# Performance work log

Hardware: AMD Instinct MI355X
Metric: run time of the kernel (lower is better)

Reference implementation:

```python
import jax, jax.numpy as jnp
import numpy as np

V = 33279   # num_tokens
E = 256     # embedding_size
H = 512     # hidden_size
NH = 8      # num_heads
L = 4       # num_layers
DH = E // NH
MAXPOS = 64


def _ln(x, g, b):
    mu = jnp.mean(x, axis=-1, keepdims=True)
    var = jnp.mean((x - mu) ** 2, axis=-1, keepdims=True)
    return (x - mu) / jnp.sqrt(var + 1e-5) * g + b


def setup_inputs() -> dict:
    key = jax.random.key(0)
    ks = jax.random.split(key, 32)
    N, S = 128, 64
    label = jax.random.randint(ks[0], (N, S), 0, V)
    # Bernoulli(0.15) BERT-style mask (deterministic stand-in for torch sampling)
    mask = (jax.random.uniform(ks[1], (N, S)) < 0.15).astype(jnp.int32)
    s = 0.02
    inp = {
        'label': label, 'mask': mask,
        'emb': jax.random.normal(ks[2], (V + 1, E)) * s,
        'pos': jax.random.normal(ks[3], (MAXPOS, E)) * s,
        'emb_g': jnp.ones((E,)), 'emb_b': jnp.zeros((E,)),
        # stacked per-layer params (leading dim L)
        'Wq': jax.random.normal(ks[4], (L, E, E)) * s, 'bq': jnp.zeros((L, E)),
        'Wk': jax.random.normal(ks[5], (L, E, E)) * s, 'bk': jnp.zeros((L, E)),
        'Wv': jax.random.normal(ks[6], (L, E, E)) * s, 'bv': jnp.zeros((L, E)),
        'Wo': jax.random.normal(ks[7], (L, E, E)) * s, 'bo': jnp.zeros((L, E)),
        'n1g': jnp.ones((L, E)), 'n1b': jnp.zeros((L, E)),
        'W1': jax.random.normal(ks[8], (L, E, H)) * s, 'b1': jnp.zeros((L, H)),
        'W2': jax.random.normal(ks[9], (L, H, E)) * s, 'b2': jnp.zeros((L, E)),
        'n2g': jnp.ones((L, E)), 'n2b': jnp.zeros((L, E)),
        # decoder head
        'dW1': jax.random.normal(ks[10], (E, E)) * s, 'db1': jnp.zeros((E,)),
        'dng': jnp.ones((E,)), 'dnb': jnp.zeros((E,)),
        'dW2': jax.random.normal(ks[11], (E, V)) * s, 'db2': jnp.zeros((V,)),
    }
    return inp


def reference(label, mask, emb, pos, emb_g, emb_b, Wq, bq, Wk, bk, Wv, bv,
              Wo, bo, n1g, n1b, W1, b1, W2, b2, n2g, n2b,
              dW1, db1, dng, dnb, dW2, db2):
    N, S = label.shape
    src_ids = jnp.where(mask == 1, V, label)  # masked-token id = num_tokens
    # embedding + positional, then LayerNorm (eval: Scaler/Dropout identity)
    x = emb[src_ids] + pos[:S][None, :, :]
    x = _ln(x, emb_g, emb_b)
    temp = jnp.asarray((E // NH) ** 0.5, x.dtype)

    def layer(x, p):
        wq, bq_, wk, bk_, wv, bv_, wo, bo_, g1, b1n, w1, b1_, w2, b2_, g2, b2n = p
        q = (x @ wq + bq_).reshape(N, S, NH, DH).transpose(0, 2, 1, 3)
        k = (x @ wk + bk_).reshape(N, S, NH, DH).transpose(0, 2, 1, 3)
        v = (x @ wv + bv_).reshape(N, S, NH, DH).transpose(0, 2, 1, 3)
        scores = jnp.einsum('nhsd,nhtd->nhst', q, k) / temp
        attn = jax.nn.softmax(scores, axis=-1)
        o = jnp.einsum('nhst,nhtd->nhsd', attn, v)
        o = o.transpose(0, 2, 1, 3).reshape(N, S, E) @ wo + bo_
        x1 = _ln(x + o, g1, b1n)
        ff = jax.nn.gelu(x1 @ w1 + b1_, approximate=False) @ w2 + b2_
        x2 = _ln(x1 + ff, g2, b2n)
        return x2, None

    x, _ = jax.lax.scan(layer, x, (Wq, bq, Wk, bk, Wv, bv, Wo, bo,
                                   n1g, n1b, W1, b1, W2, b2, n2g, n2b))
    # decoder head: linear -> gelu -> LN -> vocab projection
    h = jax.nn.gelu(x @ dW1 + db1, approximate=False)
    h = _ln(h, dng, dnb)
    logits = h @ dW2 + db2               # [N, S, V]
    logp = jax.nn.log_softmax(logits, axis=-1)
    loss = -jnp.take_along_axis(logp, label[..., None], axis=-1).mean()
    score = logits.transpose(0, 2, 1)    # [N, V, S] like torch permute(0,2,1)
    return score, loss
```

## Files before the change

### kernel.cpp

```cpp
#include <hip/hip_runtime.h>
#include <hip/hip_bf16.h>

#define DEVFN static __device__ __forceinline__

constexpr int N_ = 128, S_ = 64, T_ = N_ * S_;
constexpr int E_ = 256, H_ = 512, NH_ = 8, DH_ = 32, L_ = 4;
constexpr int V_ = 33279, VPAD_ = 33280, NVT_ = VPAD_ / 256;

typedef __attribute__((ext_vector_type(8))) short bf16x8;
typedef __attribute__((ext_vector_type(4))) float f32x4;
typedef unsigned short ushort_t;

DEVFN ushort_t f2bf(float f) {
  unsigned int u = __float_as_uint(f);
  unsigned int r = (u + 0x7fffu + ((u >> 16) & 1u)) >> 16;
  return (ushort_t)r;
}
DEVFN float bf2f(ushort_t u) { return __uint_as_float(((unsigned)u) << 16); }

DEVFN float geluf(float x) {
  return 0.5f * x * (1.f + erff(x * 0.70710678118654752440f));
}

DEVFN float wave_sum(float v) {
  #pragma unroll
  for (int off = 32; off >= 1; off >>= 1) v += __shfl_xor(v, off, 64);
  return v;
}

DEVFN float l15_sum(float v) {
  v += __shfl_xor(v, 1, 64);
  v += __shfl_xor(v, 2, 64);
  v += __shfl_xor(v, 4, 64);
  v += __shfl_xor(v, 8, 64);
  return v;
}

__global__ __launch_bounds__(256) void k_embed_ln(
    const int* __restrict__ label, const int* __restrict__ mask,
    const float* __restrict__ emb, const float* __restrict__ pos,
    const float* __restrict__ g, const float* __restrict__ b,
    float* __restrict__ x, ushort_t* __restrict__ xb) {
  int wv = threadIdx.x >> 6, lane = threadIdx.x & 63;
  int t = blockIdx.x * 4 + wv;
  int s = t & (S_ - 1);
  int id = (mask[t] == 1) ? V_ : label[t];
  int c = lane * 4;
  float4 v = *(const float4*)&emb[(size_t)id * E_ + c];
  float4 p = *(const float4*)&pos[s * E_ + c];
  v.x += p.x; v.y += p.y; v.z += p.z; v.w += p.w;
  float mean = wave_sum(v.x + v.y + v.z + v.w) * (1.f / E_);
  float4 d = {v.x - mean, v.y - mean, v.z - mean, v.w - mean};
  float var = wave_sum(d.x * d.x + d.y * d.y + d.z * d.z + d.w * d.w) * (1.f / E_);
  float rstd = 1.f / sqrtf(var + 1e-5f);
  float4 g4 = *(const float4*)&g[c];
  float4 b4 = *(const float4*)&b[c];
  float4 y = {d.x * rstd * g4.x + b4.x, d.y * rstd * g4.y + b4.y,
              d.z * rstd * g4.z + b4.z, d.w * rstd * g4.w + b4.w};
  *(float4*)&x[(size_t)t * E_ + c] = y;
  ushort4 yb = {f2bf(y.x), f2bf(y.y), f2bf(y.z), f2bf(y.w)};
  *(ushort4*)&xb[(size_t)t * E_ + c] = yb;
}

__global__ __launch_bounds__(256) void k_prep(
    const float* __restrict__ Wq, const float* __restrict__ Wk,
    const float* __restrict__ Wv, const float* __restrict__ Wo,
    const float* __restrict__ dW1, const float* __restrict__ W1,
    const float* __restrict__ W2, const float* __restrict__ bq,
    const float* __restrict__ bk, const float* __restrict__ bv,
    ushort_t* __restrict__ wqkvT, ushort_t* __restrict__ woT,
    ushort_t* __restrict__ dw1T, ushort_t* __restrict__ w1T,
    ushort_t* __restrict__ w2T, float* __restrict__ bqkv) {
  int z = blockIdx.z;
  if (z == 25) {
    if (blockIdx.x == 0 && blockIdx.y == 0) {
      for (int i = threadIdx.x; i < L_ * 768; i += 256) {
        int l = i / 768, c = i - l * 768;
        float v = (c < 256) ? bq[l * 256 + c]
                : (c < 512) ? bk[l * 256 + c - 256]
                            : bv[l * 256 + c - 512];
        bqkv[i] = v;
      }
    }
    return;
  }
  const float* src;
  ushort_t* dst;
  int K, J;
  if (z < 17) {
    if (blockIdx.x >= 8 || blockIdx.y >= 8) return;
    K = 256; J = 256;
    if (z == 16) { src = dW1; dst = dw1T; }
    else {
      int w = z >> 2, l = z & 3;
      const float* ws = (w == 0) ? Wq : (w == 1) ? Wk : (w == 2) ? Wv : Wo;
      src = ws + (size_t)l * 65536;
      dst = (w < 3) ? (wqkvT + (size_t)l * 768 * 256 + (size_t)w * 256 * 256)
                    : (woT + (size_t)l * 65536);
    }
  } else if (z < 21) {
    int l = z - 17; K = 256; J = 512;
    if (blockIdx.y >= 8) return;
    src = W1 + (size_t)l * K * J; dst = w1T + (size_t)l * J * K;
  } else {
    int l = z - 21; K = 512; J = 256;
    if (blockIdx.x >= 8) return;
    src = W2 + (size_t)l * K * J; dst = w2T + (size_t)l * J * K;
  }
  __shared__ float tile[32][33];
  int j0 = blockIdx.x * 32, k0 = blockIdx.y * 32;
  int tx = threadIdx.x & 31, ty = threadIdx.x >> 5;
  #pragma unroll
  for (int rr = 0; rr < 4; rr++) {
    int kk = ty * 4 + rr;
    tile[kk][tx] = src[(size_t)(k0 + kk) * J + j0 + tx];
  }
  __syncthreads();
  #pragma unroll
  for (int rr = 0; rr < 4; rr++) {
    int jj = ty * 4 + rr;
    dst[(size_t)(j0 + jj) * K + k0 + tx] = f2bf(tile[tx][jj]);
  }
}

template <int K, int OUT_BF16, int GELU_>
__global__ __launch_bounds__(256) void k_mm(
    const ushort_t* __restrict__ Xb, const ushort_t* __restrict__ WT,
    const float* __restrict__ bias, void* __restrict__ C, int Nout) {
  constexpr int STR = K + 8;
  __shared__ ushort_t xs[64 * STR];
  int tid = threadIdx.x, lane = tid & 63, wv = tid >> 6;
  int t0 = blockIdx.x * 64, j0 = blockIdx.y * 64;
  const ushort_t* xsrc = Xb + (size_t)t0 * K;
  for (int i = tid; i < 64 * (K / 8); i += 256) {
    int r = i / (K / 8), c = (i % (K / 8)) * 8;
    *(uint4*)&xs[r * STR + c] = *(const uint4*)&xsrc[(size_t)r * K + c];
  }
  __syncthreads();
  int l15 = lane & 15, l4 = lane >> 4;
  f32x4 acc[4] = {};
  const ushort_t* xrow = &xs[(wv * 16 + l15) * STR + l4 * 8];
  const ushort_t* wrow = WT + (size_t)j0 * K + l4 * 8;
  #pragma unroll
  for (int kb = 0; kb < K / 32; kb++) {
    bf16x8 a = *(const bf16x8*)(xrow + kb * 32);
    #pragma unroll
    for (int st = 0; st < 4; st++) {
      bf16x8 bfr = *(const bf16x8*)(wrow + (size_t)(st * 16 + l15) * K + kb * 32);
      acc[st] = __builtin_amdgcn_mfma_f32_16x16x32_bf16(a, bfr, acc[st], 0, 0, 0);
    }
  }
  #pragma unroll
  for (int st = 0; st < 4; st++) {
    int j = j0 + st * 16 + l15;
    float bv_ = bias[j];
    #pragma unroll
    for (int r = 0; r < 4; r++) {
      float val = acc[st][r] + bv_;
      if (GELU_) val = geluf(val);
      int t = t0 + wv * 16 + l4 * 4 + r;
      if (OUT_BF16)
        ((ushort_t*)C)[(size_t)t * Nout + j] = f2bf(val);
      else
        ((float*)C)[(size_t)t * Nout + j] = val;
    }
  }
}

template <int K, int GELU_PRE, int HAS_RES, int OUT_F32>
__global__ __launch_bounds__(256) void k_mm_ln2(
    const ushort_t* __restrict__ Xb, const ushort_t* __restrict__ WT,
    const float* __restrict__ bias, const float* __restrict__ res,
    const float* __restrict__ g, const float* __restrict__ bet,
    float* __restrict__ y, ushort_t* __restrict__ yb) {
  constexpr int STR = K + 8;
  __shared__ ushort_t xs[16 * STR];
  __shared__ float redA[4][16], redB[4][16];
  int tid = threadIdx.x, lane = tid & 63, wv = tid >> 6;
  int t0 = blockIdx.x * 16;
  const ushort_t* xsrc = Xb + (size_t)t0 * K;
  for (int i = tid; i < 16 * (K / 8); i += 256) {
    int r = i / (K / 8), c = (i % (K / 8)) * 8;
    *(uint4*)&xs[r * STR + c] = *(const uint4*)&xsrc[(size_t)r * K + c];
  }
  __syncthreads();
  int l15 = lane & 15, l4 = lane >> 4;
  f32x4 acc[4] = {};
  const ushort_t* xrow = &xs[l15 * STR + l4 * 8];
  const ushort_t* wrow = WT + (size_t)(wv * 64) * K + l4 * 8;
  #pragma unroll
  for (int kb = 0; kb < K / 32; kb++) {
    bf16x8 a = *(const bf16x8*)(xrow + kb * 32);
    #pragma unroll
    for (int st = 0; st < 4; st++) {
      bf16x8 bfr = *(const bf16x8*)(wrow + (size_t)(st * 16 + l15) * K + kb * 32);
      acc[st] = __builtin_amdgcn_mfma_f32_16x16x32_bf16(a, bfr, acc[st], 0, 0, 0);
    }
  }
  float val[4][4];
  #pragma unroll
  for (int st = 0; st < 4; st++) {
    int j = wv * 64 + st * 16 + l15;
    float bv_ = bias[j];
    #pragma unroll
    for (int r = 0; r < 4; r++) {
      float v = acc[st][r] + bv_;
      if (GELU_PRE) v = geluf(v);
      if (HAS_RES) v += res[(size_t)(t0 + l4 * 4 + r) * E_ + j];
      val[st][r] = v;
    }
  }
  #pragma unroll
  for (int r = 0; r < 4; r++) {
    float s = val[0][r] + val[1][r] + val[2][r] + val[3][r];
    s = l15_sum(s);
    if (l15 == 0) redA[wv][l4 * 4 + r] = s;
  }
  __syncthreads();
  float mean[4];
  #pragma unroll
  for (int r = 0; r < 4; r++) {
    int row = l4 * 4 + r;
    mean[r] = (redA[0][row] + redA[1][row] + redA[2][row] + redA[3][row]) * (1.f / E_);
  }
  #pragma unroll
  for (int r = 0; r < 4; r++) {
    float s = 0.f;
    #pragma unroll
    for (int st = 0; st < 4; st++) {
      float d = val[st][r] - mean[r];
      s += d * d;
    }
    s = l15_sum(s);
    if (l15 == 0) redB[wv][l4 * 4 + r] = s;
  }
  __syncthreads();
  float rstd[4];
  #pragma unroll
  for (int r = 0; r < 4; r++) {
    int row = l4 * 4 + r;
    float var = (redB[0][row] + redB[1][row] + redB[2][row] + redB[3][row]) * (1.f / E_);
    rstd[r] = 1.f / sqrtf(var + 1e-5f);
  }
  #pragma unroll
  for (int st = 0; st < 4; st++) {
    int j = wv * 64 + st * 16 + l15;
    float gj = g[j], bj = bet[j];
    #pragma unroll
    for (int r = 0; r < 4; r++) {
      int t = t0 + l4 * 4 + r;
      float o = (val[st][r] - mean[r]) * rstd[r] * gj + bj;
      if (OUT_F32) y[(size_t)t * E_ + j] = o;
      yb[(size_t)t * E_ + j] = f2bf(o);
    }
  }
}

__global__ __launch_bounds__(256) void k_ff(
    const ushort_t* __restrict__ Xb, const ushort_t* __restrict__ W1T,
    const float* __restrict__ b1v, const ushort_t* __restrict__ W2T,
    const float* __restrict__ b2v, const float* __restrict__ res,
    const float* __restrict__ g, const float* __restrict__ bet,
    float* __restrict__ y, ushort_t* __restrict__ yb) {
  __shared__ ushort_t xs[16 * 264];
  __shared__ ushort_t hsd[16 * 520];
  __shared__ float redA[4][16], redB[4][16];
  int tid = threadIdx.x, lane = tid & 63, wv = tid >> 6;
  int t0 = blockIdx.x * 16;
  const ushort_t* xsrc = Xb + (size_t)t0 * E_;
  for (int i = tid; i < 16 * 32; i += 256) {
    int r = i >> 5, c = (i & 31) * 8;
    *(uint4*)&xs[r * 264 + c] = *(const uint4*)&xsrc[(size_t)r * E_ + c];
  }
  __syncthreads();
  int l15 = lane & 15, l4 = lane >> 4;
  f32x4 acc1[8] = {};
  const ushort_t* xrow = &xs[l15 * 264 + l4 * 8];
  const ushort_t* w1r = W1T + (size_t)(wv * 128) * E_ + l4 * 8;
  #pragma unroll
  for (int kb = 0; kb < 8; kb++) {
    bf16x8 a = *(const bf16x8*)(xrow + kb * 32);
    #pragma unroll
    for (int ht = 0; ht < 8; ht++) {
      bf16x8 b = *(const bf16x8*)(w1r + (size_t)(ht * 16 + l15) * E_ + kb * 32);
      acc1[ht] = __builtin_amdgcn_mfma_f32_16x16x32_bf16(a, b, acc1[ht], 0, 0, 0);
    }
  }
  #pragma unroll
  for (int ht = 0; ht < 8; ht++) {
    int hc = wv * 128 + ht * 16 + l15;
    float bv_ = b1v[hc];
    #pragma unroll
    for (int r = 0; r < 4; r++) {
      float v = geluf(acc1[ht][r] + bv_);
      hsd[(l4 * 4 + r) * 520 + hc] = f2bf(v);
    }
  }
  __syncthreads();
  f32x4 acc2[4] = {};
  const ushort_t* hrow = &hsd[l15 * 520 + l4 * 8];
  const ushort_t* w2r = W2T + (size_t)(wv * 64) * H_ + l4 * 8;
  #pragma unroll
  for (int kb = 0; kb < 16; kb++) {
    bf16x8 a = *(const bf16x8*)(hrow + kb * 32);
    #pragma unroll
    for (int st = 0; st < 4; st++) {
      bf16x8 b = *(const bf16x8*)(w2r + (size_t)(st * 16 + l15) * H_ + kb * 32);
      acc2[st] = __builtin_amdgcn_mfma_f32_16x16x32_bf16(a, b, acc2[st], 0, 0, 0);
    }
  }
  float val[4][4];
  #pragma unroll
  for (int st = 0; st < 4; st++) {
    int j = wv * 64 + st * 16 + l15;
    float bv_ = b2v[j];
    #pragma unroll
    for (int r = 0; r < 4; r++)
      val[st][r] = acc2[st][r] + bv_ + res[(size_t)(t0 + l4 * 4 + r) * E_ + j];
  }
  #pragma unroll
  for (int r = 0; r < 4; r++) {
    float s = val[0][r] + val[1][r] + val[2][r] + val[3][r];
    s = l15_sum(s);
    if (l15 == 0) redA[wv][l4 * 4 + r] = s;
  }
  __syncthreads();
  float mean[4];
  #pragma unroll
  for (int r = 0; r < 4; r++) {
    int row = l4 * 4 + r;
    mean[r] = (redA[0][row] + redA[1][row] + redA[2][row] + redA[3][row]) * (1.f / E_);
  }
  #pragma unroll
  for (int r = 0; r < 4; r++) {
    float s = 0.f;
    #pragma unroll
    for (int st = 0; st < 4; st++) {
      float d = val[st][r] - mean[r];
      s += d * d;
    }
    s = l15_sum(s);
    if (l15 == 0) redB[wv][l4 * 4 + r] = s;
  }
  __syncthreads();
  float rstd[4];
  #pragma unroll
  for (int r = 0; r < 4; r++) {
    int row = l4 * 4 + r;
    float var = (redB[0][row] + redB[1][row] + redB[2][row] + redB[3][row]) * (1.f / E_);
    rstd[r] = 1.f / sqrtf(var + 1e-5f);
  }
  #pragma unroll
  for (int st = 0; st < 4; st++) {
    int j = wv * 64 + st * 16 + l15;
    float gj = g[j], bj = bet[j];
    #pragma unroll
    for (int r = 0; r < 4; r++) {
      int t = t0 + l4 * 4 + r;
      float o = (val[st][r] - mean[r]) * rstd[r] * gj + bj;
      y[(size_t)t * E_ + j] = o;
      yb[(size_t)t * E_ + j] = f2bf(o);
    }
  }
}

__global__ __launch_bounds__(256) void k_attn(
    const ushort_t* __restrict__ qkv, ushort_t* __restrict__ o) {
  __shared__ __align__(16) ushort_t vt_[32 * 72];
  __shared__ __align__(16) ushort_t ps[64 * 72];
  int n = blockIdx.x >> 3, h = blockIdx.x & 7;
  int tid = threadIdx.x, lane = tid & 63, wv = tid >> 6;
  int l15 = lane & 15, l4 = lane >> 4;
  const ushort_t* qbase = qkv + (size_t)n * S_ * 768 + h * DH_;
  for (int i = tid; i < S_ * DH_; i += 256) {
    int t = i >> 5, d = i & 31;
    vt_[d * 72 + t] = qbase[(size_t)t * 768 + 512 + d];
  }
  int srow = wv * 16 + l15;
  bf16x8 aq = *(const bf16x8*)&qbase[(size_t)srow * 768 + l4 * 8];
  f32x4 sc[4];
  #pragma unroll
  for (int st = 0; st < 4; st++) {
    bf16x8 bk_ = *(const bf16x8*)&qbase[(size_t)(st * 16 + l15) * 768 + 256 + l4 * 8];
    f32x4 z = {};
    sc[st] = __builtin_amdgcn_mfma_f32_16x16x32_bf16(aq, bk_, z, 0, 0, 0);
  }
  const float scale = 0.17677669529663687f;
  #pragma unroll
  for (int st = 0; st < 4; st++)
    #pragma unroll
    for (int r = 0; r < 4; r++) sc[st][r] *= scale;
  #pragma unroll
  for (int r = 0; r < 4; r++) {
    float m = fmaxf(fmaxf(sc[0][r], sc[1][r]), fmaxf(sc[2][r], sc[3][r]));
    m = fmaxf(m, __shfl_xor(m, 1, 64));
    m = fmaxf(m, __shfl_xor(m, 2, 64));
    m = fmaxf(m, __shfl_xor(m, 4, 64));
    m = fmaxf(m, __shfl_xor(m, 8, 64));
    float p0 = __expf(sc[0][r] - m), p1 = __expf(sc[1][r] - m);
    float p2 = __expf(sc[2][r] - m), p3 = __expf(sc[3][r] - m);
    float sum = p0 + p1 + p2 + p3;
    sum += __shfl_xor(sum, 1, 64);
    sum += __shfl_xor(sum, 2, 64);
    sum += __shfl_xor(sum, 4, 64);
    sum += __shfl_xor(sum, 8, 64);
    float inv = 1.f / sum;
    int prow = (wv * 16 + l4 * 4 + r) * 72;
    ps[prow + 0 * 16 + l15] = f2bf(p0 * inv);
    ps[prow + 1 * 16 + l15] = f2bf(p1 * inv);
    ps[prow + 2 * 16 + l15] = f2bf(p2 * inv);
    ps[prow + 3 * 16 + l15] = f2bf(p3 * inv);
  }
  __syncthreads();
  f32x4 oc[2] = {};
  #pragma unroll
  for (int kb = 0; kb < 2; kb++) {
    bf16x8 ap = *(const bf16x8*)&ps[srow * 72 + kb * 32 + l4 * 8];
    #pragma unroll
    for (int st2 = 0; st2 < 2; st2++) {
      bf16x8 bv_ = *(const bf16x8*)&vt_[(st2 * 16 + l15) * 72 + kb * 32 + l4 * 8];
      oc[st2] = __builtin_amdgcn_mfma_f32_16x16x32_bf16(ap, bv_, oc[st2], 0, 0, 0);
    }
  }
  ushort_t* ob = o + (size_t)n * S_ * E_ + h * DH_;
  #pragma unroll
  for (int st2 = 0; st2 < 2; st2++)
    #pragma unroll
    for (int r = 0; r < 4; r++)
      ob[(size_t)(wv * 16 + l4 * 4 + r) * E_ + st2 * 16 + l15] = f2bf(oc[st2][r]);
}

__global__ __launch_bounds__(256) void k_w2t(const float* __restrict__ w,
                                             ushort_t* __restrict__ wt) {
  __shared__ float tile[32 * 33];
  int tx = threadIdx.x & 31, ty = threadIdx.x >> 5;
  int v0 = blockIdx.x * 32, k0 = blockIdx.y * 32;
  #pragma unroll
  for (int rr = 0; rr < 4; rr++) {
    int kk = ty * 4 + rr;
    int vv = v0 + tx;
    tile[kk * 33 + tx] = (vv < V_) ? w[(size_t)(k0 + kk) * V_ + vv] : 0.f;
  }
  __syncthreads();
  #pragma unroll
  for (int rr = 0; rr < 4; rr++) {
    int vv = ty * 4 + rr;
    wt[(size_t)(v0 + vv) * E_ + k0 + tx] = f2bf(tile[tx * 33 + vv]);
  }
}

__global__ __launch_bounds__(256) void k_vocab(
    const ushort_t* __restrict__ hbf, const ushort_t* __restrict__ wt,
    const float* __restrict__ db2, float* __restrict__ out,
    float* __restrict__ pmax, float* __restrict__ psum) {
  __shared__ ushort_t hs[64 * 264];
  __shared__ float redm[4][64];
  __shared__ float reds[4][64];
  int n = blockIdx.x, vt = blockIdx.y;
  int tid = threadIdx.x, lane = tid & 63, wv = tid >> 6;
  const ushort_t* hsrc = hbf + (size_t)n * S_ * E_;
  for (int i = tid; i < (S_ * E_) / 8; i += 256) {
    int s = i >> 5, kc = (i & 31) * 8;
    *(uint4*)&hs[s * 264 + kc] = *(const uint4*)&hsrc[s * E_ + kc];
  }
  __syncthreads();
  int l15 = lane & 15, l4 = lane >> 4;
  float rm[4], rs[4];
  #pragma unroll
  for (int st = 0; st < 4; st++) { rm[st] = -INFINITY; rs[st] = 0.f; }
  #pragma unroll
  for (int h2 = 0; h2 < 2; h2++) {
    const ushort_t* Ap0 =
        wt + (size_t)(vt * 256 + h2 * 128 + wv * 16 + l15) * E_ + l4 * 8;
    const ushort_t* Ap1 = Ap0 + (size_t)64 * E_;
    f32x4 acc[2][4] = {};
    #pragma unroll
    for (int kb = 0; kb < 8; kb++) {
      bf16x8 a0 = *(const bf16x8*)(Ap0 + kb * 32);
      bf16x8 a1 = *(const bf16x8*)(Ap1 + kb * 32);
      #pragma unroll
      for (int st = 0; st < 4; st++) {
        bf16x8 bfr = *(const bf16x8*)&hs[(st * 16 + l15) * 264 + kb * 32 + l4 * 8];
        acc[0][st] = __builtin_amdgcn_mfma_f32_16x16x32_bf16(a0, bfr, acc[0][st], 0, 0, 0);
        acc[1][st] = __builtin_amdgcn_mfma_f32_16x16x32_bf16(a1, bfr, acc[1][st], 0, 0, 0);
      }
    }
    float vals[2][4][4];
    #pragma unroll
    for (int mt = 0; mt < 2; mt++) {
      #pragma unroll
      for (int j = 0; j < 4; j++) {
        int v = vt * 256 + h2 * 128 + wv * 16 + mt * 64 + l4 * 4 + j;
        bool valid = v < V_;
        float bias = valid ? db2[v] : 0.f;
        size_t ob = ((size_t)n * V_ + v) * S_;
        #pragma unroll
        for (int st = 0; st < 4; st++) {
          float val = valid ? (acc[mt][st][j] + bias) : -INFINITY;
          vals[mt][st][j] = val;
          if (valid) __builtin_nontemporal_store(val, &out[ob + st * 16 + l15]);
        }
      }
    }
    #pragma unroll
    for (int st = 0; st < 4; st++) {
      float m = -INFINITY;
      #pragma unroll
      for (int mt = 0; mt < 2; mt++)
        #pragma unroll
        for (int j = 0; j < 4; j++) m = fmaxf(m, vals[mt][st][j]);
      m = fmaxf(m, __shfl_xor(m, 16, 64));
      m = fmaxf(m, __shfl_xor(m, 32, 64));
      float sum = 0.f;
      #pragma unroll
      for (int mt = 0; mt < 2; mt++)
        #pragma unroll
        for (int j = 0; j < 4; j++) sum += __expf(vals[mt][st][j] - m);
      sum += __shfl_xor(sum, 16, 64);
      sum += __shfl_xor(sum, 32, 64);
      float nm = fmaxf(rm[st], m);
      rs[st] = rs[st] * __expf(rm[st] - nm) + sum * __expf(m - nm);
      rm[st] = nm;
    }
  }
  if (l4 == 0) {
    #pragma unroll
    for (int st = 0; st < 4; st++) {
      redm[wv][st * 16 + l15] = rm[st];
      reds[wv][st * 16 + l15] = rs[st];
    }
  }
  __syncthreads();
  if (wv == 0 && l4 == 0) {
    #pragma unroll
    for (int st = 0; st < 4; st++) {
      int s = st * 16 + l15;
      float M = fmaxf(fmaxf(redm[0][s], redm[1][s]), fmaxf(redm[2][s], redm[3][s]));
      float Sa = reds[0][s] * __expf(redm[0][s] - M) +
                 reds[1][s] * __expf(redm[1][s] - M) +
                 reds[2][s] * __expf(redm[2][s] - M) +
                 reds[3][s] * __expf(redm[3][s] - M);
      size_t pi = ((size_t)n * NVT_ + vt) * S_ + s;
      pmax[pi] = M;
      psum[pi] = Sa;
    }
  }
}

__global__ __launch_bounds__(512) void k_lossf(
    const float* __restrict__ pmax, const float* __restrict__ psum,
    const float* __restrict__ out, const int* __restrict__ label,
    float* __restrict__ partial) {
  __shared__ float sm[512], ssum[512];
  int n = blockIdx.x, tid = threadIdx.x;
  int s = tid & 63, qq = tid >> 6;
  float m = -INFINITY, sum = 0.f;
  for (int vt = qq; vt < NVT_; vt += 8) {
    size_t pi = ((size_t)n * NVT_ + vt) * S_ + s;
    float m2 = pmax[pi], s2 = psum[pi];
    float nm = fmaxf(m, m2);
    sum = sum * __expf(m - nm) + s2 * __expf(m2 - nm);
    m = nm;
  }
  sm[tid] = m; ssum[tid] = sum;
  __syncthreads();
  if (qq == 0) {
    float M = sm[s], Sa = ssum[s];
    #pragma unroll
    for (int p = 1; p < 8; p++) {
      float m2 = sm[p * 64 + s], s2 = ssum[p * 64 + s];
      float nm = fmaxf(M, m2);
      Sa = Sa * __expf(M - nm) + s2 * __expf(m2 - nm);
      M = nm;
    }
    float lse = M + logf(Sa);
    int lab = label[n * S_ + s];
    float lx = out[((size_t)n * V_ + lab) * S_ + s];
    partial[n * S_ + s] = lse - lx;
  }
}

__global__ __launch_bounds__(256) void k_loss2(const float* __restrict__ partial,
                                               float* __restrict__ dst) {
  __shared__ float sbuf[4];
  int tid = threadIdx.x;
  float acc = 0.f;
  for (int i = tid; i < T_; i += 256) acc += partial[i];
  #pragma unroll
  for (int off = 32; off >= 1; off >>= 1) acc += __shfl_xor(acc, off, 64);
  int lane = tid & 63, wid = tid >> 6;
  if (lane == 0) sbuf[wid] = acc;
  __syncthreads();
  if (tid == 0) dst[0] = (sbuf[0] + sbuf[1] + sbuf[2] + sbuf[3]) / (float)T_;
}

extern "C" void kernel_launch(void* const* d_in, const int* in_sizes, int n_in,
                              void* d_out, int out_size, void* d_ws, size_t ws_size,
                              hipStream_t stream) {
  const int*   label = (const int*)d_in[0];
  const int*   mask  = (const int*)d_in[1];
  const float* emb   = (const float*)d_in[2];
  const float* pos   = (const float*)d_in[3];
  const float* emb_g = (const float*)d_in[4];
  const float* emb_b = (const float*)d_in[5];
  const float* Wq  = (const float*)d_in[6];
  const float* bq  = (const float*)d_in[7];
  const float* Wk  = (const float*)d_in[8];
  const float* bk  = (const float*)d_in[9];
  const float* Wv  = (const float*)d_in[10];
  const float* bv  = (const float*)d_in[11];
  const float* Wo  = (const float*)d_in[12];
  const float* bo  = (const float*)d_in[13];
  const float* n1g = (const float*)d_in[14];
  const float* n1b = (const float*)d_in[15];
  const float* W1  = (const float*)d_in[16];
  const float* b1  = (const float*)d_in[17];
  const float* W2  = (const float*)d_in[18];
  const float* b2  = (const float*)d_in[19];
  const float* n2g = (const float*)d_in[20];
  const float* n2b = (const float*)d_in[21];
  const float* dW1 = (const float*)d_in[22];
  const float* db1 = (const float*)d_in[23];
  const float* dng = (const float*)d_in[24];
  const float* dnb = (const float*)d_in[25];
  const float* dW2 = (const float*)d_in[26];
  const float* db2 = (const float*)d_in[27];
  float* out = (float*)d_out;
  (void)in_sizes; (void)n_in; (void)out_size; (void)ws_size;

  char* base = (char*)d_ws;
  size_t off = 0;
  auto alloc = [&](size_t bytes) {
    char* p = base + off;
    off += (bytes + 255) & ~(size_t)255;
    return p;
  };
  float*    x    = (float*)alloc((size_t)T_ * E_ * 4);
  ushort_t* xb   = (ushort_t*)alloc((size_t)T_ * E_ * 2);
  float*    x1   = (float*)alloc((size_t)T_ * E_ * 4);
  ushort_t* x1b  = (ushort_t*)alloc((size_t)T_ * E_ * 2);
  ushort_t* qkv  = (ushort_t*)alloc((size_t)T_ * 768 * 2);
  ushort_t* obuf = (ushort_t*)alloc((size_t)T_ * E_ * 2);
  ushort_t* wqkvT = (ushort_t*)alloc((size_t)L_ * 768 * E_ * 2);
  ushort_t* woT   = (ushort_t*)alloc((size_t)L_ * E_ * E_ * 2);
  ushort_t* w1T   = (ushort_t*)alloc((size_t)L_ * H_ * E_ * 2);
  ushort_t* w2T   = (ushort_t*)alloc((size_t)L_ * E_ * H_ * 2);
  ushort_t* dw1T  = (ushort_t*)alloc((size_t)E_ * E_ * 2);
  ushort_t* wt    = (ushort_t*)alloc((size_t)VPAD_ * E_ * 2);
  float*    bqkv  = (float*)alloc((size_t)L_ * 768 * 4);
  float*    partial = (float*)alloc((size_t)T_ * 4);
  ushort_t* hbf = obuf;
  float* pmax = x;
  float* psum = pmax + (size_t)N_ * NVT_ * S_;

  k_prep<<<dim3(16, 16, 26), 256, 0, stream>>>(Wq, Wk, Wv, Wo, dW1, W1, W2,
                                               bq, bk, bv, wqkvT, woT, dw1T,
                                               w1T, w2T, bqkv);
  k_w2t<<<dim3(VPAD_ / 32, E_ / 32), 256, 0, stream>>>(dW2, wt);

  k_embed_ln<<<T_ / 4, 256, 0, stream>>>(label, mask, emb, pos, emb_g, emb_b, x, xb);

  for (int l = 0; l < L_; l++) {
    k_mm<E_, 1, 0><<<dim3(T_ / 64, 12), 256, 0, stream>>>(
        xb, wqkvT + (size_t)l * 768 * E_, bqkv + l * 768, qkv, 768);
    k_attn<<<N_ * NH_, 256, 0, stream>>>(qkv, obuf);
    k_mm_ln2<E_, 0, 1, 1><<<T_ / 16, 256, 0, stream>>>(
        obuf, woT + (size_t)l * E_ * E_, bo + l * E_, x,
        n1g + l * E_, n1b + l * E_, x1, x1b);
    k_ff<<<T_ / 16, 256, 0, stream>>>(
        x1b, w1T + (size_t)l * H_ * E_, b1 + l * H_,
        w2T + (size_t)l * E_ * H_, b2 + l * E_, x1,
        n2g + l * E_, n2b + l * E_, x, xb);
  }

  k_mm_ln2<E_, 1, 0, 0><<<T_ / 16, 256, 0, stream>>>(
      xb, dw1T, db1, nullptr, dng, dnb, nullptr, hbf);

  k_vocab<<<dim3(N_, NVT_), 256, 0, stream>>>(hbf, wt, db2, out, pmax, psum);

  k_lossf<<<N_, 512, 0, stream>>>(pmax, psum, out, label, partial);
  k_loss2<<<1, 256, 0, stream>>>(partial, out + (size_t)N_ * V_ * S_);
}
```

Baseline: 850.1 us.

## Fuse QKV projection into per-head attention kernel

Replaces the separate QKV GEMM and attention kernels with one kernel per (batch, head) block. Each block loads that batch's 64 token rows, computes its head's Q, K and V with MFMA into shared memory, then runs softmax attention, so the QKV intermediate never goes to global memory and one launch per layer disappears. It also reuses the x staging buffer for the probability tile and drops a barrier before the PV product, since each wave only reads the rows it wrote. The cost is that the eight head-blocks of a batch each reload the same activation rows and each computes only a narrow 96-column projection.

```diff
diff --git a/kernel.cpp b/kernel.cpp
--- a/kernel.cpp
+++ b/kernel.cpp
@@ -2,6 +2,7 @@
 #include <hip/hip_bf16.h>
 
 #define DEVFN static __device__ __forceinline__
+#define MFMA16(a, b, c) __builtin_amdgcn_mfma_f32_16x16x32_bf16((a), (b), (c), 0, 0, 0)
 
 constexpr int N_ = 128, S_ = 64, T_ = N_ * S_;
 constexpr int E_ = 256, H_ = 512, NH_ = 8, DH_ = 32, L_ = 4;
@@ -123,273 +124,70 @@
   }
 }
 
-template <int K, int OUT_BF16, int GELU_>
-__global__ __launch_bounds__(256) void k_mm(
-    const ushort_t* __restrict__ Xb, const ushort_t* __restrict__ WT,
-    const float* __restrict__ bias, void* __restrict__ C, int Nout) {
-  constexpr int STR = K + 8;
-  __shared__ ushort_t xs[64 * STR];
-  int tid = threadIdx.x, lane = tid & 63, wv = tid >> 6;
-  int t0 = blockIdx.x * 64, j0 = blockIdx.y * 64;
-  const ushort_t* xsrc = Xb + (size_t)t0 * K;
-  for (int i = tid; i < 64 * (K / 8); i += 256) {
-    int r = i / (K / 8), c = (i % (K / 8)) * 8;
-    *(uint4*)&xs[r * STR + c] = *(const uint4*)&xsrc[(size_t)r * K + c];
-  }
-  __syncthreads();
-  int l15 = lane & 15, l4 = lane >> 4;
-  f32x4 acc[4] = {};
-  const ushort_t* xrow = &xs[(wv * 16 + l15) * STR + l4 * 8];
-  const ushort_t* wrow = WT + (size_t)j0 * K + l4 * 8;
-  #pragma unroll
-  for (int kb = 0; kb < K / 32; kb++) {
-    bf16x8 a = *(const bf16x8*)(xrow + kb * 32);
-    #pragma unroll
-    for (int st = 0; st < 4; st++) {
-      bf16x8 bfr = *(const bf16x8*)(wrow + (size_t)(st * 16 + l15) * K + kb * 32);
-      acc[st] = __builtin_amdgcn_mfma_f32_16x16x32_bf16(a, bfr, acc[st], 0, 0, 0);
-    }
-  }
-  #pragma unroll
-  for (int st = 0; st < 4; st++) {
-    int j = j0 + st * 16 + l15;
-    float bv_ = bias[j];
-    #pragma unroll
-    for (int r = 0; r < 4; r++) {
-      float val = acc[st][r] + bv_;
-      if (GELU_) val = geluf(val);
-      int t = t0 + wv * 16 + l4 * 4 + r;
-      if (OUT_BF16)
-        ((ushort_t*)C)[(size_t)t * Nout + j] = f2bf(val);
-      else
-        ((float*)C)[(size_t)t * Nout + j] = val;
-    }
-  }
-}
-
-template <int K, int GELU_PRE, int HAS_RES, int OUT_F32>
-__global__ __launch_bounds__(256) void k_mm_ln2(
-    const ushort_t* __restrict__ Xb, const ushort_t* __restrict__ WT,
-    const float* __restrict__ bias, const float* __restrict__ res,
-    const float* __restrict__ g, const float* __restrict__ bet,
-    float* __restrict__ y, ushort_t* __restrict__ yb) {
-  constexpr int STR = K + 8;
-  __shared__ ushort_t xs[16 * STR];
-  __shared__ float redA[4][16], redB[4][16];
-  int tid = threadIdx.x, lane = tid & 63, wv = tid >> 6;
-  int t0 = blockIdx.x * 16;
-  const ushort_t* xsrc = Xb + (size_t)t0 * K;
-  for (int i = tid; i < 16 * (K / 8); i += 256) {
-    int r = i / (K / 8), c = (i % (K / 8)) * 8;
-    *(uint4*)&xs[r * STR + c] = *(const uint4*)&xsrc[(size_t)r * K + c];
-  }
-  __syncthreads();
-  int l15 = lane & 15, l4 = lane >> 4;
-  f32x4 acc[4] = {};
-  const ushort_t* xrow = &xs[l15 * STR + l4 * 8];
-  const ushort_t* wrow = WT + (size_t)(wv * 64) * K + l4 * 8;
-  #pragma unroll
-  for (int kb = 0; kb < K / 32; kb++) {
-    bf16x8 a = *(const bf16x8*)(xrow + kb * 32);
-    #pragma unroll
-    for (int st = 0; st < 4; st++) {
-      bf16x8 bfr = *(const bf16x8*)(wrow + (size_t)(st * 16 + l15) * K + kb * 32);
-      acc[st] = __builtin_amdgcn_mfma_f32_16x16x32_bf16(a, bfr, acc[st], 0, 0, 0);
-    }
-  }
-  float val[4][4];
-  #pragma unroll
-  for (int st = 0; st < 4; st++) {
-    int j = wv * 64 + st * 16 + l15;
-    float bv_ = bias[j];
-    #pragma unroll
-    for (int r = 0; r < 4; r++) {
-      float v = acc[st][r] + bv_;
-      if (GELU_PRE) v = geluf(v);
-      if (HAS_RES) v += res[(size_t)(t0 + l4 * 4 + r) * E_ + j];
-      val[st][r] = v;
-    }
-  }
-  #pragma unroll
-  for (int r = 0; r < 4; r++) {
-    float s = val[0][r] + val[1][r] + val[2][r] + val[3][r];
-    s = l15_sum(s);
-    if (l15 == 0) redA[wv][l4 * 4 + r] = s;
-  }
-  __syncthreads();
-  float mean[4];
-  #pragma unroll
-  for (int r = 0; r < 4; r++) {
-    int row = l4 * 4 + r;
-    mean[r] = (redA[0][row] + redA[1][row] + redA[2][row] + redA[3][row]) * (1.f / E_);
-  }
-  #pragma unroll
-  for (int r = 0; r < 4; r++) {
-    float s = 0.f;
-    #pragma unroll
-    for (int st = 0; st < 4; st++) {
-      float d = val[st][r] - mean[r];
-      s += d * d;
-    }
-    s = l15_sum(s);
-    if (l15 == 0) redB[wv][l4 * 4 + r] = s;
-  }
-  __syncthreads();
-  float rstd[4];
-  #pragma unroll
-  for (int r = 0; r < 4; r++) {
-    int row = l4 * 4 + r;
-    float var = (redB[0][row] + redB[1][row] + redB[2][row] + redB[3][row]) * (1.f / E_);
-    rstd[r] = 1.f / sqrtf(var + 1e-5f);
-  }
-  #pragma unroll
-  for (int st = 0; st < 4; st++) {
-    int j = wv * 64 + st * 16 + l15;
-    float gj = g[j], bj = bet[j];
-    #pragma unroll
-    for (int r = 0; r < 4; r++) {
-      int t = t0 + l4 * 4 + r;
-      float o = (val[st][r] - mean[r]) * rstd[r] * gj + bj;
-      if (OUT_F32) y[(size_t)t * E_ + j] = o;
-      yb[(size_t)t * E_ + j] = f2bf(o);
-    }
-  }
-}
-
-__global__ __launch_bounds__(256) void k_ff(
-    const ushort_t* __restrict__ Xb, const ushort_t* __restrict__ W1T,
-    const float* __restrict__ b1v, const ushort_t* __restrict__ W2T,
-    const float* __restrict__ b2v, const float* __restrict__ res,
-    const float* __restrict__ g, const float* __restrict__ bet,
-    float* __restrict__ y, ushort_t* __restrict__ yb) {
-  __shared__ ushort_t xs[16 * 264];
-  __shared__ ushort_t hsd[16 * 520];
-  __shared__ float redA[4][16], redB[4][16];
-  int tid = threadIdx.x, lane = tid & 63, wv = tid >> 6;
-  int t0 = blockIdx.x * 16;
-  const ushort_t* xsrc = Xb + (size_t)t0 * E_;
-  for (int i = tid; i < 16 * 32; i += 256) {
-    int r = i >> 5, c = (i & 31) * 8;
-    *(uint4*)&xs[r * 264 + c] = *(const uint4*)&xsrc[(size_t)r * E_ + c];
-  }
-  __syncthreads();
-  int l15 = lane & 15, l4 = lane >> 4;
-  f32x4 acc1[8] = {};
-  const ushort_t* xrow = &xs[l15 * 264 + l4 * 8];
-  const ushort_t* w1r = W1T + (size_t)(wv * 128) * E_ + l4 * 8;
-  #pragma unroll
-  for (int kb = 0; kb < 8; kb++) {
-    bf16x8 a = *(const bf16x8*)(xrow + kb * 32);
-    #pragma unroll
-    for (int ht = 0; ht < 8; ht++) {
-      bf16x8 b = *(const bf16x8*)(w1r + (size_t)(ht * 16 + l15) * E_ + kb * 32);
-      acc1[ht] = __builtin_amdgcn_mfma_f32_16x16x32_bf16(a, b, acc1[ht], 0, 0, 0);
-    }
-  }
-  #pragma unroll
-  for (int ht = 0; ht < 8; ht++) {
-    int hc = wv * 128 + ht * 16 + l15;
-    float bv_ = b1v[hc];
-    #pragma unroll
-    for (int r = 0; r < 4; r++) {
-      float v = geluf(acc1[ht][r] + bv_);
-      hsd[(l4 * 4 + r) * 520 + hc] = f2bf(v);
-    }
-  }
-  __syncthreads();
-  f32x4 acc2[4] = {};
-  const ushort_t* hrow = &hsd[l15 * 520 + l4 * 8];
-  const ushort_t* w2r = W2T + (size_t)(wv * 64) * H_ + l4 * 8;
-  #pragma unroll
-  for (int kb = 0; kb < 16; kb++) {
-    bf16x8 a = *(const bf16x8*)(hrow + kb * 32);
-    #pragma unroll
-    for (int st = 0; st < 4; st++) {
-      bf16x8 b = *(const bf16x8*)(w2r + (size_t)(st * 16 + l15) * H_ + kb * 32);
-      acc2[st] = __builtin_amdgcn_mfma_f32_16x16x32_bf16(a, b, acc2[st], 0, 0, 0);
-    }
-  }
-  float val[4][4];
-  #pragma unroll
-  for (int st = 0; st < 4; st++) {
-    int j = wv * 64 + st * 16 + l15;
-    float bv_ = b2v[j];
-    #pragma unroll
-    for (int r = 0; r < 4; r++)
-      val[st][r] = acc2[st][r] + bv_ + res[(size_t)(t0 + l4 * 4 + r) * E_ + j];
-  }
-  #pragma unroll
-  for (int r = 0; r < 4; r++) {
-    float s = val[0][r] + val[1][r] + val[2][r] + val[3][r];
-    s = l15_sum(s);
-    if (l15 == 0) redA[wv][l4 * 4 + r] = s;
-  }
-  __syncthreads();
-  float mean[4];
-  #pragma unroll
-  for (int r = 0; r < 4; r++) {
-    int row = l4 * 4 + r;
-    mean[r] = (redA[0][row] + redA[1][row] + redA[2][row] + redA[3][row]) * (1.f / E_);
-  }
-  #pragma unroll
-  for (int r = 0; r < 4; r++) {
-    float s = 0.f;
-    #pragma unroll
-    for (int st = 0; st < 4; st++) {
-      float d = val[st][r] - mean[r];
-      s += d * d;
-    }
-    s = l15_sum(s);
-    if (l15 == 0) redB[wv][l4 * 4 + r] = s;
-  }
-  __syncthreads();
-  float rstd[4];
-  #pragma unroll
-  for (int r = 0; r < 4; r++) {
-    int row = l4 * 4 + r;
-    float var = (redB[0][row] + redB[1][row] + redB[2][row] + redB[3][row]) * (1.f / E_);
-    rstd[r] = 1.f / sqrtf(var + 1e-5f);
-  }
-  #pragma unroll
-  for (int st = 0; st < 4; st++) {
-    int j = wv * 64 + st * 16 + l15;
-    float gj = g[j], bj = bet[j];
-    #pragma unroll
-    for (int r = 0; r < 4; r++) {
-      int t = t0 + l4 * 4 + r;
-      float o = (val[st][r] - mean[r]) * rstd[r] * gj + bj;
-      y[(size_t)t * E_ + j] = o;
-      yb[(size_t)t * E_ + j] = f2bf(o);
-    }
-  }
-}
-
-__global__ __launch_bounds__(256) void k_attn(
-    const ushort_t* __restrict__ qkv, ushort_t* __restrict__ o) {
+__global__ __launch_bounds__(256) void k_qa(
+    const ushort_t* __restrict__ xb, const ushort_t* __restrict__ wqkvT_l,
+    const float* __restrict__ bqkv_l, ushort_t* __restrict__ o) {
+  __shared__ __align__(16) ushort_t xs[64 * 264];
+  __shared__ __align__(16) ushort_t qs[64 * 40];
+  __shared__ __align__(16) ushort_t ks[64 * 40];
   __shared__ __align__(16) ushort_t vt_[32 * 72];
-  __shared__ __align__(16) ushort_t ps[64 * 72];
   int n = blockIdx.x >> 3, h = blockIdx.x & 7;
   int tid = threadIdx.x, lane = tid & 63, wv = tid >> 6;
   int l15 = lane & 15, l4 = lane >> 4;
-  const ushort_t* qbase = qkv + (size_t)n * S_ * 768 + h * DH_;
-  for (int i = tid; i < S_ * DH_; i += 256) {
-    int t = i >> 5, d = i & 31;
-    vt_[d * 72 + t] = qbase[(size_t)t * 768 + 512 + d];
-  }
+  const ushort_t* xsrc = xb + (size_t)n * S_ * E_;
+  for (int i = tid; i < 64 * 32; i += 256) {
+    int r = i >> 5, c = (i & 31) * 8;
+    *(uint4*)&xs[r * 264 + c] = *(const uint4*)&xsrc[(size_t)r * E_ + c];
+  }
+  __syncthreads();
+  const ushort_t* xrow = &xs[(wv * 16 + l15) * 264 + l4 * 8];
+  const ushort_t* wq = wqkvT_l + (size_t)(h * 32) * E_ + l4 * 8;
+  const ushort_t* wk = wqkvT_l + (size_t)(256 + h * 32) * E_ + l4 * 8;
+  const ushort_t* wvp = wqkvT_l + (size_t)(512 + h * 32) * E_ + l4 * 8;
+  f32x4 qa[2] = {}, ka[2] = {}, va[2] = {};
+  #pragma unroll
+  for (int kb = 0; kb < 8; kb++) {
+    bf16x8 a = *(const bf16x8*)(xrow + kb * 32);
+    #pragma unroll
+    for (int st = 0; st < 2; st++) {
+      bf16x8 bq_ = *(const bf16x8*)(wq + (size_t)(st * 16 + l15) * E_ + kb * 32);
+      bf16x8 bk_ = *(const bf16x8*)(wk + (size_t)(st * 16 + l15) * E_ + kb * 32);
+      bf16x8 bv_ = *(const bf16x8*)(wvp + (size_t)(st * 16 + l15) * E_ + kb * 32);
+      qa[st] = MFMA16(a, bq_, qa[st]);
+      ka[st] = MFMA16(a, bk_, ka[st]);
+      va[st] = MFMA16(a, bv_, va[st]);
+    }
+  }
+  #pragma unroll
+  for (int st = 0; st < 2; st++) {
+    int c = st * 16 + l15;
+    float bqv = bqkv_l[h * 32 + c];
+    float bkv = bqkv_l[256 + h * 32 + c];
+    float bvv = bqkv_l[512 + h * 32 + c];
+    #pragma unroll
+    for (int r = 0; r < 4; r++) {
+      int t = wv * 16 + l4 * 4 + r;
+      qs[t * 40 + c] = f2bf(qa[st][r] + bqv);
+      ks[t * 40 + c] = f2bf(ka[st][r] + bkv);
+      vt_[c * 72 + t] = f2bf(va[st][r] + bvv);
+    }
+  }
+  __syncthreads();
   int srow = wv * 16 + l15;
-  bf16x8 aq = *(const bf16x8*)&qbase[(size_t)srow * 768 + l4 * 8];
+  bf16x8 aq = *(const bf16x8*)&qs[srow * 40 + l4 * 8];
   f32x4 sc[4];
   #pragma unroll
   for (int st = 0; st < 4; st++) {
-    bf16x8 bk_ = *(const bf16x8*)&qbase[(size_t)(st * 16 + l15) * 768 + 256 + l4 * 8];
+    bf16x8 bk_ = *(const bf16x8*)&ks[(st * 16 + l15) * 40 + l4 * 8];
     f32x4 z = {};
-    sc[st] = __builtin_amdgcn_mfma_f32_16x16x32_bf16(aq, bk_, z, 0, 0, 0);
+    sc[st] = MFMA16(aq, bk_, z);
   }
   const float scale = 0.17677669529663687f;
   #pragma unroll
   for (int st = 0; st < 4; st++)
     #pragma unroll
     for (int r = 0; r < 4; r++) sc[st][r] *= scale;
+  ushort_t* ps = xs;
   #pragma unroll
   for (int r = 0; r < 4; r++) {
     float m = fmaxf(fmaxf(sc[0][r], sc[1][r]), fmaxf(sc[2][r], sc[3][r]));
@@ -411,7 +209,6 @@
     ps[prow + 2 * 16 + l15] = f2bf(p2 * inv);
     ps[prow + 3 * 16 + l15] = f2bf(p3 * inv);
   }
-  __syncthreads();
   f32x4 oc[2] = {};
   #pragma unroll
   for (int kb = 0; kb < 2; kb++) {
@@ -419,7 +216,7 @@
     #pragma unroll
     for (int st2 = 0; st2 < 2; st2++) {
       bf16x8 bv_ = *(const bf16x8*)&vt_[(st2 * 16 + l15) * 72 + kb * 32 + l4 * 8];
-      oc[st2] = __builtin_amdgcn_mfma_f32_16x16x32_bf16(ap, bv_, oc[st2], 0, 0, 0);
+      oc[st2] = MFMA16(ap, bv_, oc[st2]);
     }
   }
   ushort_t* ob = o + (size_t)n * S_ * E_ + h * DH_;
@@ -428,6 +225,203 @@
     #pragma unroll
     for (int r = 0; r < 4; r++)
       ob[(size_t)(wv * 16 + l4 * 4 + r) * E_ + st2 * 16 + l15] = f2bf(oc[st2][r]);
+}
+
+template <int K, int GELU_PRE, int HAS_RES, int OUT_F32>
+__global__ __launch_bounds__(256) void k_mm_ln2(
+    const ushort_t* __restrict__ Xb, const ushort_t* __restrict__ WT,
+    const float* __restrict__ bias, const float* __restrict__ res,
+    const float* __restrict__ g, const float* __restrict__ bet,
+    float* __restrict__ y, ushort_t* __restrict__ yb) {
+  constexpr int STR = K + 8;
+  __shared__ ushort_t xs[16 * STR];
+  __shared__ float redA[4][16], redB[4][16];
+  int tid = threadIdx.x, lane = tid & 63, wv = tid >> 6;
+  int t0 = blockIdx.x * 16;
+  const ushort_t* xsrc = Xb + (size_t)t0 * K;
+  for (int i = tid; i < 16 * (K / 8); i += 256) {
+    int r = i / (K / 8), c = (i % (K / 8)) * 8;
+    *(uint4*)&xs[r * STR + c] = *(const uint4*)&xsrc[(size_t)r * K + c];
+  }
+  __syncthreads();
+  int l15 = lane & 15, l4 = lane >> 4;
+  f32x4 acc[4] = {};
+  const ushort_t* xrow = &xs[l15 * STR + l4 * 8];
+  const ushort_t* wrow = WT + (size_t)(wv * 64) * K + l4 * 8;
+  #pragma unroll
+  for (int kb = 0; kb < K / 32; kb++) {
+    bf16x8 a = *(const bf16x8*)(xrow + kb * 32);
+    #pragma unroll
+    for (int st = 0; st < 4; st++) {
+      bf16x8 bfr = *(const bf16x8*)(wrow + (size_t)(st * 16 + l15) * K + kb * 32);
+      acc[st] = MFMA16(a, bfr, acc[st]);
+    }
+  }
+  float val[4][4];
+  #pragma unroll
+  for (int st = 0; st < 4; st++) {
+    int j = wv * 64 + st * 16 + l15;
+    float bv_ = bias[j];
+    #pragma unroll
+    for (int r = 0; r < 4; r++) {
+      float v = acc[st][r] + bv_;
+      if (GELU_PRE) v = geluf(v);
+      if (HAS_RES) v += res[(size_t)(t0 + l4 * 4 + r) * E_ + j];
+      val[st][r] = v;
+    }
+  }
+  #pragma unroll
+  for (int r = 0; r < 4; r++) {
+    float s = val[0][r] + val[1][r] + val[2][r] + val[3][r];
+    s = l15_sum(s);
+    if (l15 == 0) redA[wv][l4 * 4 + r] = s;
+  }
+  __syncthreads();
+  float mean[4];
+  #pragma unroll
+  for (int r = 0; r < 4; r++) {
+    int row = l4 * 4 + r;
+    mean[r] = (redA[0][row] + redA[1][row] + redA[2][row] + redA[3][row]) * (1.f / E_);
+  }
+  #pragma unroll
+  for (int r = 0; r < 4; r++) {
+    float s = 0.f;
+    #pragma unroll
+    for (int st = 0; st < 4; st++) {
+      float d = val[st][r] - mean[r];
+      s += d * d;
+    }
+    s = l15_sum(s);
+    if (l15 == 0) redB[wv][l4 * 4 + r] = s;
+  }
+  __syncthreads();
+  float rstd[4];
+  #pragma unroll
+  for (int r = 0; r < 4; r++) {
+    int row = l4 * 4 + r;
+    float var = (redB[0][row] + redB[1][row] + redB[2][row] + redB[3][row]) * (1.f / E_);
+    rstd[r] = 1.f / sqrtf(var + 1e-5f);
+  }
+  #pragma unroll
+  for (int st = 0; st < 4; st++) {
+    int j = wv * 64 + st * 16 + l15;
+    float gj = g[j], bj = bet[j];
+    #pragma unroll
+    for (int r = 0; r < 4; r++) {
+      int t = t0 + l4 * 4 + r;
+      float o = (val[st][r] - mean[r]) * rstd[r] * gj + bj;
+      if (OUT_F32) y[(size_t)t * E_ + j] = o;
+      yb[(size_t)t * E_ + j] = f2bf(o);
+    }
+  }
+}
+
+__global__ __launch_bounds__(256) void k_ff(
+    const ushort_t* __restrict__ Xb, const ushort_t* __restrict__ W1T,
+    const float* __restrict__ b1v, const ushort_t* __restrict__ W2T,
+    const float* __restrict__ b2v, const float* __restrict__ res,
+    const float* __restrict__ g, const float* __restrict__ bet,
+    float* __restrict__ y, ushort_t* __restrict__ yb) {
+  __shared__ ushort_t xs[16 * 264];
+  __shared__ ushort_t hsd[16 * 520];
+  __shared__ float redA[4][16], redB[4][16];
+  int tid = threadIdx.x, lane = tid & 63, wv = tid >> 6;
+  int t0 = blockIdx.x * 16;
+  const ushort_t* xsrc = Xb + (size_t)t0 * E_;
+  for (int i = tid; i < 16 * 32; i += 256) {
+    int r = i >> 5, c = (i & 31) * 8;
+    *(uint4*)&xs[r * 264 + c] = *(const uint4*)&xsrc[(size_t)r * E_ + c];
+  }
+  __syncthreads();
+  int l15 = lane & 15, l4 = lane >> 4;
+  f32x4 acc1[8] = {};
+  const ushort_t* xrow = &xs[l15 * 264 + l4 * 8];
+  const ushort_t* w1r = W1T + (size_t)(wv * 128) * E_ + l4 * 8;
+  #pragma unroll
+  for (int kb = 0; kb < 8; kb++) {
+    bf16x8 a = *(const bf16x8*)(xrow + kb * 32);
+    #pragma unroll
+    for (int ht = 0; ht < 8; ht++) {
+      bf16x8 b = *(const bf16x8*)(w1r + (size_t)(ht * 16 + l15) * E_ + kb * 32);
+      acc1[ht] = MFMA16(a, b, acc1[ht]);
+    }
+  }
+  #pragma unroll
+  for (int ht = 0; ht < 8; ht++) {
+    int hc = wv * 128 + ht * 16 + l15;
+    float bv_ = b1v[hc];
+    #pragma unroll
+    for (int r = 0; r < 4; r++) {
+      float v = geluf(acc1[ht][r] + bv_);
+      hsd[(l4 * 4 + r) * 520 + hc] = f2bf(v);
+    }
+  }
+  __syncthreads();
+  f32x4 acc2[4] = {};
+  const ushort_t* hrow = &hsd[l15 * 520 + l4 * 8];
+  const ushort_t* w2r = W2T + (size_t)(wv * 64) * H_ + l4 * 8;
+  #pragma unroll
+  for (int kb = 0; kb < 16; kb++) {
+    bf16x8 a = *(const bf16x8*)(hrow + kb * 32);
+    #pragma unroll
+    for (int st = 0; st < 4; st++) {
+      bf16x8 b = *(const bf16x8*)(w2r + (size_t)(st * 16 + l15) * H_ + kb * 32);
+      acc2[st] = MFMA16(a, b, acc2[st]);
+    }
+  }
+  float val[4][4];
+  #pragma unroll
+  for (int st = 0; st < 4; st++) {
+    int j = wv * 64 + st * 16 + l15;
+    float bv_ = b2v[j];
+    #pragma unroll
+    for (int r = 0; r < 4; r++)
+      val[st][r] = acc2[st][r] + bv_ + res[(size_t)(t0 + l4 * 4 + r) * E_ + j];
+  }
+  #pragma unroll
+  for (int r = 0; r < 4; r++) {
+    float s = val[0][r] + val[1][r] + val[2][r] + val[3][r];
+    s = l15_sum(s);
+    if (l15 == 0) redA[wv][l4 * 4 + r] = s;
+  }
+  __syncthreads();
+  float mean[4];
+  #pragma unroll
+  for (int r = 0; r < 4; r++) {
+    int row = l4 * 4 + r;
+    mean[r] = (redA[0][row] + redA[1][row] + redA[2][row] + redA[3][row]) * (1.f / E_);
+  }
+  #pragma unroll
+  for (int r = 0; r < 4; r++) {
+    float s = 0.f;
+    #pragma unroll
+    for (int st = 0; st < 4; st++) {
+      float d = val[st][r] - mean[r];
+      s += d * d;
+    }
+    s = l15_sum(s);
+    if (l15 == 0) redB[wv][l4 * 4 + r] = s;
+  }
+  __syncthreads();
+  float rstd[4];
+  #pragma unroll
+  for (int r = 0; r < 4; r++) {
+    int row = l4 * 4 + r;
+    float var = (redB[0][row] + redB[1][row] + redB[2][row] + redB[3][row]) * (1.f / E_);
+    rstd[r] = 1.f / sqrtf(var + 1e-5f);
+  }
+  #pragma unroll
+  for (int st = 0; st < 4; st++) {
+    int j = wv * 64 + st * 16 + l15;
+    float gj = g[j], bj = bet[j];
+    #pragma unroll
+    for (int r = 0; r < 4; r++) {
+      int t = t0 + l4 * 4 + r;
+      float o = (val[st][r] - mean[r]) * rstd[r] * gj + bj;
+      y[(size_t)t * E_ + j] = o;
+      yb[(size_t)t * E_ + j] = f2bf(o);
+    }
+  }
 }
 
 __global__ __launch_bounds__(256) void k_w2t(const float* __restrict__ w,
@@ -481,8 +475,8 @@
       #pragma unroll
       for (int st = 0; st < 4; st++) {
         bf16x8 bfr = *(const bf16x8*)&hs[(st * 16 + l15) * 264 + kb * 32 + l4 * 8];
-        acc[0][st] = __builtin_amdgcn_mfma_f32_16x16x32_bf16(a0, bfr, acc[0][st], 0, 0, 0);
-        acc[1][st] = __builtin_amdgcn_mfma_f32_16x16x32_bf16(a1, bfr, acc[1][st], 0, 0, 0);
+        acc[0][st] = MFMA16(a0, bfr, acc[0][st]);
+        acc[1][st] = MFMA16(a1, bfr, acc[1][st]);
       }
     }
     float vals[2][4][4];
@@ -639,7 +633,6 @@
   ushort_t* xb   = (ushort_t*)alloc((size_t)T_ * E_ * 2);
   float*    x1   = (float*)alloc((size_t)T_ * E_ * 4);
   ushort_t* x1b  = (ushort_t*)alloc((size_t)T_ * E_ * 2);
-  ushort_t* qkv  = (ushort_t*)alloc((size_t)T_ * 768 * 2);
   ushort_t* obuf = (ushort_t*)alloc((size_t)T_ * E_ * 2);
   ushort_t* wqkvT = (ushort_t*)alloc((size_t)L_ * 768 * E_ * 2);
   ushort_t* woT   = (ushort_t*)alloc((size_t)L_ * E_ * E_ * 2);
@@ -661,9 +654,8 @@
   k_embed_ln<<<T_ / 4, 256, 0, stream>>>(label, mask, emb, pos, emb_g, emb_b, x, xb);
 
   for (int l = 0; l < L_; l++) {
-    k_mm<E_, 1, 0><<<dim3(T_ / 64, 12), 256, 0, stream>>>(
-        xb, wqkvT + (size_t)l * 768 * E_, bqkv + l * 768, qkv, 768);
-    k_attn<<<N_ * NH_, 256, 0, stream>>>(qkv, obuf);
+    k_qa<<<N_ * NH_, 256, 0, stream>>>(
+        xb, wqkvT + (size_t)l * 768 * E_, bqkv + l * 768, obuf);
     k_mm_ln2<E_, 0, 1, 1><<<T_ / 16, 256, 0, stream>>>(
         obuf, woT + (size_t)l * E_ * E_, bo + l * E_, x,
         n1g + l * E_, n1b + l * E_, x1, x1b);
```

Result: faster. 827.4 us (-2.7%).
